# Kernel optimization log

Hardware: AMD Instinct MI355X
Metric: run time of the kernel (lower is better)

The kernel has to match this reference:

```python
import jax, jax.numpy as jnp
import numpy as np

N_NODES = 50000
N_EDGES = 600000
D = 128
EDGE_D = 32
N_LAYERS = 3
BN_EPS = 1e-5


def setup_inputs() -> dict:
    key = jax.random.key(0)
    ks = jax.random.split(key, 8)
    x = jax.random.normal(ks[0], (N_NODES, D), dtype=jnp.float32)
    edge_index = jax.random.randint(ks[1], (2, N_EDGES), 0, N_NODES, dtype=jnp.int64)
    edge_attr = jax.random.normal(ks[2], (N_EDGES, EDGE_D), dtype=jnp.float32)
    W_lin = jax.random.normal(ks[3], (N_LAYERS, EDGE_D, D), dtype=jnp.float32) * 0.05
    b_lin = jnp.zeros((N_LAYERS, D), dtype=jnp.float32)
    W1 = jax.random.normal(ks[4], (N_LAYERS, D, D), dtype=jnp.float32) * 0.05
    b1 = jnp.zeros((N_LAYERS, D), dtype=jnp.float32)
    W2 = jax.random.normal(ks[5], (N_LAYERS, D, D), dtype=jnp.float32) * 0.05
    b2 = jnp.zeros((N_LAYERS, D), dtype=jnp.float32)
    gamma = jnp.ones((N_LAYERS, D), dtype=jnp.float32)
    beta = jnp.zeros((N_LAYERS, D), dtype=jnp.float32)
    return {"x": x, "edge_index": edge_index, "edge_attr": edge_attr,
            "W_lin": W_lin, "b_lin": b_lin, "W1": W1, "b1": b1,
            "W2": W2, "b2": b2, "gamma": gamma, "beta": beta}


def reference(x, edge_index, edge_attr, W_lin, b_lin, W1, b1, W2, b2, gamma, beta):
    # MPNN with GINEConv layers: for each layer,
    #   msg_e = ReLU(x[src_e] + Linear(edge_attr_e))      (PyG GINEConv edge lift)
    #   agg_i = sum over edges with dst==i of msg_e        (scatter-sum)
    #   h     = MLP((1+eps)*x + agg), eps=0
    #   x     = ReLU(BatchNorm1d(h))                       (training-mode batch stats)
    src, dst = edge_index[0], edge_index[1]
    n = x.shape[0]
    for l in range(W1.shape[0]):
        e = edge_attr @ W_lin[l] + b_lin[l]                 # [E, D]
        msg = jax.nn.relu(x[src] + e)                       # gather + fuse
        agg = jax.ops.segment_sum(msg, dst, num_segments=n)  # [N, D]
        h = x + agg                                         # eps = 0
        h = jax.nn.relu(h @ W1[l] + b1[l]) @ W2[l] + b2[l]   # GIN MLP
        mu = jnp.mean(h, axis=0)
        var = jnp.var(h, axis=0)
        h = (h - mu) * jax.lax.rsqrt(var + BN_EPS) * gamma[l] + beta[l]
        x = jax.nn.relu(h)
    return x
```

## Files before the change

kernel.cpp:

```cpp
#include <hip/hip_runtime.h>

#define D_DIM 128
#define EDGE_DIM 32
#define BN_EPS 1e-5f

typedef __attribute__((ext_vector_type(8))) _Float16 f16x8;
typedef __attribute__((ext_vector_type(2))) _Float16 half2v;
typedef __attribute__((ext_vector_type(4))) float f32x4;
typedef unsigned short ushort_t;

__device__ __forceinline__ unsigned short f2h(float f) {
    union { _Float16 h; unsigned short u; } c;
    c.h = (_Float16)f;
    return c.u;
}
__device__ __forceinline__ unsigned pk2h(float lo, float hi) {
    return (unsigned)f2h(lo) | ((unsigned)f2h(hi) << 16);
}
__device__ __forceinline__ half2v asH2(unsigned u) {
    union { unsigned u; half2v h; } c;
    c.u = u;
    return c.h;
}
__device__ __forceinline__ float fdot2f(half2v a, half2v b, float c) {
#if __has_builtin(__builtin_amdgcn_fdot2)
    return __builtin_amdgcn_fdot2(a, b, c, false);
#else
    return c + (float)a.x * (float)b.x + (float)a.y * (float)b.y;
#endif
}

__global__ __launch_bounds__(256) void hist_kernel(
    const int* __restrict__ dst, int* __restrict__ cnt, int E)
{
    for (int e = blockIdx.x * 256 + threadIdx.x; e < E; e += gridDim.x * 256)
        atomicAdd(&cnt[dst[e]], 1);
}

__global__ __launch_bounds__(256) void scan_local_kernel(
    const int* __restrict__ cnt, int* __restrict__ off,
    int* __restrict__ blksum, int n)
{
    __shared__ int part[256];
    const int t = threadIdx.x;
    const int base = blockIdx.x * 2048 + t * 8;
    int v[8];
    int s = 0;
#pragma unroll
    for (int j = 0; j < 8; ++j) {
        const int idx = base + j;
        const int c = (idx < n) ? cnt[idx] : 0;
        v[j] = s;
        s += c;
    }
    part[t] = s;
    __syncthreads();
    for (int d = 1; d < 256; d <<= 1) {
        const int val = (t >= d) ? part[t - d] : 0;
        __syncthreads();
        part[t] += val;
        __syncthreads();
    }
    const int texcl = (t > 0) ? part[t - 1] : 0;
#pragma unroll
    for (int j = 0; j < 8; ++j) {
        const int idx = base + j;
        if (idx < n) off[idx] = texcl + v[j];
    }
    if (t == 255) blksum[blockIdx.x] = part[255];
}

__global__ __launch_bounds__(64) void scan_tops_kernel(
    int* __restrict__ blksum, int* __restrict__ off, int n, int B)
{
    if (threadIdx.x == 0) {
        int run = 0;
        for (int b = 0; b < B; ++b) {
            const int v = blksum[b];
            blksum[b] = run;
            run += v;
        }
        off[n] = run;
    }
}

__global__ __launch_bounds__(256) void scan_add_kernel(
    int* __restrict__ off, int* __restrict__ cur,
    const int* __restrict__ blksum, int n)
{
    const int base = blockIdx.x * 2048;
    const int add = blksum[blockIdx.x];
    for (int j = threadIdx.x; j < 2048; j += 256) {
        const int i = base + j;
        if (i < n) {
            const int v = off[i] + add;
            off[i] = v;
            cur[i] = v;
        }
    }
}

__global__ __launch_bounds__(256) void scatter_conv_kernel(
    const int* __restrict__ src, const int* __restrict__ dst,
    const float* __restrict__ ea,
    int* __restrict__ cur, int* __restrict__ srcs,
    uint4* __restrict__ ea16q, int E)
{
    for (int e = blockIdx.x * 256 + threadIdx.x; e < E; e += gridDim.x * 256) {
        const int p = atomicAdd(&cur[dst[e]], 1);
        srcs[p] = src[e];
        const float* __restrict__ er = ea + (size_t)e * EDGE_DIM;
#pragma unroll
        for (int q = 0; q < 4; ++q) {
            const float4 a = *(const float4*)(er + q * 8);
            const float4 b = *(const float4*)(er + q * 8 + 4);
            uint4 o;
            o.x = pk2h(a.x, a.y); o.y = pk2h(a.z, a.w);
            o.z = pk2h(b.x, b.y); o.w = pk2h(b.z, b.w);
            ea16q[(size_t)p * 4 + q] = o;
        }
    }
}

__global__ __launch_bounds__(256) void wl_build_kernel(
    const float* __restrict__ Wl, unsigned* __restrict__ wl16d)
{
#pragma unroll
    for (int r = 0; r < 8; ++r) {
        const int idx = r * 256 + threadIdx.x;
        const int kp = idx >> 7, c = idx & 127;
        wl16d[idx] = pk2h(Wl[(2 * kp) * D_DIM + c], Wl[(2 * kp + 1) * D_DIM + c]);
    }
}

__global__ __launch_bounds__(256) void xprep0_kernel(
    const float* __restrict__ h, uint2* __restrict__ x16q, int M)
{
    const int total = M * 32;
    for (int i = blockIdx.x * 256 + threadIdx.x; i < total; i += gridDim.x * 256) {
        const float4 v = ((const float4*)h)[i];
        uint2 o; o.x = pk2h(v.x, v.y); o.y = pk2h(v.z, v.w);
        x16q[i] = o;
    }
}

template<int OUTF32>
__global__ __launch_bounds__(256) void apply_kernel(
    const ushort_t* __restrict__ h16, const float* __restrict__ scsh,
    uint2* __restrict__ x16q, float* __restrict__ outp, int M)
{
    __shared__ float sc[128], sh[128];
    if (threadIdx.x < 128) {
        sc[threadIdx.x] = scsh[threadIdx.x];
        sh[threadIdx.x] = scsh[128 + threadIdx.x];
    }
    __syncthreads();
    const int total = M * 32;
    for (int i = blockIdx.x * 256 + threadIdx.x; i < total; i += gridDim.x * 256) {
        const uint2 hv = *(const uint2*)(h16 + (size_t)i * 4);
        const half2v a = asH2(hv.x), b = asH2(hv.y);
        const int c = (i & 31) * 4;
        const float v0 = fmaxf(fmaf((float)a.x, sc[c + 0], sh[c + 0]), 0.f);
        const float v1 = fmaxf(fmaf((float)a.y, sc[c + 1], sh[c + 1]), 0.f);
        const float v2 = fmaxf(fmaf((float)b.x, sc[c + 2], sh[c + 2]), 0.f);
        const float v3 = fmaxf(fmaf((float)b.y, sc[c + 3], sh[c + 3]), 0.f);
        if (OUTF32) {
            f32x4 o = {v0, v1, v2, v3};
            *(f32x4*)(outp + (size_t)i * 4) = o;
        } else {
            uint2 o; o.x = pk2h(v0, v1); o.y = pk2h(v2, v3);
            x16q[i] = o;
        }
    }
}

__global__ __launch_bounds__(256, 2) void edge_agg_kernel(
    const unsigned* __restrict__ x16d,
    const int*      __restrict__ srcs,
    const uint4*    __restrict__ ea16q,
    const int*      __restrict__ row_off,
    const unsigned* __restrict__ wl16d,
    const float*    __restrict__ bl,
    float*          __restrict__ agg,
    int nNodes)
{
    const int lane = threadIdx.x & 63;
    const int wid  = threadIdx.x >> 6;

    unsigned wA[16], wB[16];
#pragma unroll
    for (int kp = 0; kp < 16; ++kp) {
        const uint2 w2 = *(const uint2*)(wl16d + kp * 128 + 2 * lane);
        wA[kp] = w2.x; wB[kp] = w2.y;
    }
#pragma unroll
    for (int kp = 0; kp < 16; ++kp) {
        asm volatile("" : "+v"(wA[kp]));
        asm volatile("" : "+v"(wB[kp]));
    }
    const float b0 = bl[2 * lane];
    const float b1 = bl[2 * lane + 1];

    const int stride = gridDim.x * 4;
    for (int node = blockIdx.x * 4 + wid; node < nNodes; node += stride) {
        const int beg = __builtin_amdgcn_readfirstlane(row_off[node]);
        const int end = __builtin_amdgcn_readfirstlane(row_off[node + 1]);
        float acc0 = 0.f, acc1 = 0.f;

        const int nPair = (end - beg) >> 1;
        int j = beg;
        int sA = 0, sB = 0;
        if (nPair > 0) { sA = srcs[j]; sB = srcs[j + 1]; }

#pragma unroll 1
        for (int it = 0; it < nPair; ++it) {
            const unsigned xdA = x16d[(size_t)sA * 64 + lane];
            const unsigned xdB = x16d[(size_t)sB * 64 + lane];
            int sA2 = sA, sB2 = sB;
            if (it + 1 < nPair) {
                sA2 = srcs[j + 2];
                sB2 = srcs[j + 3];
            }
            const uint4 a0 = ea16q[(size_t)j * 4 + 0];
            const uint4 a1 = ea16q[(size_t)j * 4 + 1];
            const uint4 a2 = ea16q[(size_t)j * 4 + 2];
            const uint4 a3 = ea16q[(size_t)j * 4 + 3];
            const uint4 c0 = ea16q[(size_t)(j + 1) * 4 + 0];
            const uint4 c1 = ea16q[(size_t)(j + 1) * 4 + 1];
            const uint4 c2 = ea16q[(size_t)(j + 1) * 4 + 2];
            const uint4 c3 = ea16q[(size_t)(j + 1) * 4 + 3];

            const unsigned awA[16] = {a0.x, a0.y, a0.z, a0.w,
                                      a1.x, a1.y, a1.z, a1.w,
                                      a2.x, a2.y, a2.z, a2.w,
                                      a3.x, a3.y, a3.z, a3.w};
            const unsigned awB[16] = {c0.x, c0.y, c0.z, c0.w,
                                      c1.x, c1.y, c1.z, c1.w,
                                      c2.x, c2.y, c2.z, c2.w,
                                      c3.x, c3.y, c3.z, c3.w};
            float pA0 = b0, pA1 = b1, pB0 = b0, pB1 = b1;
            float qA0 = 0.f, qA1 = 0.f, qB0 = 0.f, qB1 = 0.f;
#pragma unroll
            for (int kp = 0; kp < 8; ++kp) {
                pA0 = fdot2f(asH2(awA[kp]), asH2(wA[kp]), pA0);
                pA1 = fdot2f(asH2(awA[kp]), asH2(wB[kp]), pA1);
                pB0 = fdot2f(asH2(awB[kp]), asH2(wA[kp]), pB0);
                pB1 = fdot2f(asH2(awB[kp]), asH2(wB[kp]), pB1);
                qA0 = fdot2f(asH2(awA[kp + 8]), asH2(wA[kp + 8]), qA0);
                qA1 = fdot2f(asH2(awA[kp + 8]), asH2(wB[kp + 8]), qA1);
                qB0 = fdot2f(asH2(awB[kp + 8]), asH2(wA[kp + 8]), qB0);
                qB1 = fdot2f(asH2(awB[kp + 8]), asH2(wB[kp + 8]), qB1);
            }
            const half2v xhA = asH2(xdA);
            const half2v xhB = asH2(xdB);
            acc0 += fmaxf((float)xhA.x + pA0 + qA0, 0.f)
                  + fmaxf((float)xhB.x + pB0 + qB0, 0.f);
            acc1 += fmaxf((float)xhA.y + pA1 + qA1, 0.f)
                  + fmaxf((float)xhB.y + pB1 + qB1, 0.f);
            sA = sA2; sB = sB2;
            j += 2;
        }
        if (j < end) {
            const int s = srcs[j];
            const unsigned xd = x16d[(size_t)s * 64 + lane];
            const uint4 a0 = ea16q[(size_t)j * 4 + 0];
            const uint4 a1 = ea16q[(size_t)j * 4 + 1];
            const uint4 a2 = ea16q[(size_t)j * 4 + 2];
            const uint4 a3 = ea16q[(size_t)j * 4 + 3];
            const unsigned aw[16] = {a0.x, a0.y, a0.z, a0.w,
                                     a1.x, a1.y, a1.z, a1.w,
                                     a2.x, a2.y, a2.z, a2.w,
                                     a3.x, a3.y, a3.z, a3.w};
            float p0 = b0, p1 = b1, q0 = 0.f, q1 = 0.f;
#pragma unroll
            for (int kp = 0; kp < 8; ++kp) {
                p0 = fdot2f(asH2(aw[kp]), asH2(wA[kp]), p0);
                p1 = fdot2f(asH2(aw[kp]), asH2(wB[kp]), p1);
                q0 = fdot2f(asH2(aw[kp + 8]), asH2(wA[kp + 8]), q0);
                q1 = fdot2f(asH2(aw[kp + 8]), asH2(wB[kp + 8]), q1);
            }
            const half2v xh = asH2(xd);
            acc0 += fmaxf((float)xh.x + p0 + q0, 0.f);
            acc1 += fmaxf((float)xh.y + p1 + q1, 0.f);
        }
        *(float2*)(agg + (size_t)node * D_DIM + 2 * lane) = make_float2(acc0, acc1);
    }
}

__global__ __launch_bounds__(256) void fused_mlp_kernel(
    const unsigned* __restrict__ x16d,
    const float* __restrict__ agg,
    const float* __restrict__ W1,
    const float* __restrict__ b1,
    const float* __restrict__ W2,
    const float* __restrict__ b2,
    ushort_t* __restrict__ h16,
    float* __restrict__ sums,
    int M)
{
    __shared__ char ATb[128 * 256];
    __shared__ char WTb[128 * 256];
    __shared__ float bsum[256];
    const int tid = threadIdx.x;
    const int m0  = blockIdx.x * 128;

    bsum[tid] = 0.f;

#pragma unroll
    for (int i = 0; i < 16; ++i) {
        const int idx = i * 256 + tid;
        const int r = idx >> 5, c4 = idx & 31;
        const int row = m0 + r;
        f32x4 v = {0.f, 0.f, 0.f, 0.f};
        if (row < M) {
            const uint2 xv = *(const uint2*)(x16d + (size_t)row * 64 + c4 * 2);
            const f32x4 g  = *(const f32x4*)(agg + (size_t)row * 128 + c4 * 4);
            const half2v xa = asH2(xv.x), xb = asH2(xv.y);
            v[0] = (float)xa.x + g[0];
            v[1] = (float)xa.y + g[1];
            v[2] = (float)xb.x + g[2];
            v[3] = (float)xb.y + g[3];
        }
        uint2 p; p.x = pk2h(v[0], v[1]); p.y = pk2h(v[2], v[3]);
        *(uint2*)(ATb + r * 256 + ((c4 * 8) ^ ((r & 7) << 4))) = p;
    }
#pragma unroll
    for (int i = 0; i < 8; ++i) {
        const int c4 = (tid >> 6) + 4 * i;
        const int kp = tid & 63;
        const f32x4 wa = *(const f32x4*)(W1 + (size_t)(2 * kp) * 128 + c4 * 4);
        const f32x4 wb = *(const f32x4*)(W1 + (size_t)(2 * kp + 1) * 128 + c4 * 4);
#pragma unroll
        for (int j = 0; j < 4; ++j) {
            const int col = c4 * 4 + j;
            *(unsigned*)(WTb + col * 256 + ((kp * 4) ^ ((col & 7) << 4))) = pk2h(wa[j], wb[j]);
        }
    }
    __syncthreads();

    const int lane = tid & 63;
    const int w    = tid >> 6;
    const int fr   = lane & 15;
    const int fg   = lane >> 4;
    const int ar0  = w * 32 + fr;
    const int asz  = (ar0 & 7) << 4;

    f32x4 acc[2][8];
#pragma unroll
    for (int a = 0; a < 2; ++a)
#pragma unroll
        for (int b = 0; b < 8; ++b) acc[a][b] = (f32x4){0.f, 0.f, 0.f, 0.f};

#pragma unroll
    for (int ks = 0; ks < 4; ++ks) {
        const int kb = ks * 64 + fg * 16;
        const f16x8 a0 = *(const f16x8*)(ATb + ar0 * 256 + (kb ^ asz));
        const f16x8 a1 = *(const f16x8*)(ATb + (ar0 + 16) * 256 + (kb ^ asz));
#pragma unroll
        for (int cb = 0; cb < 8; ++cb) {
            const int col = cb * 16 + fr;
            const f16x8 b = *(const f16x8*)(WTb + col * 256 + (kb ^ ((col & 7) << 4)));
            acc[0][cb] = __builtin_amdgcn_mfma_f32_16x16x32_f16(a0, b, acc[0][cb], 0, 0, 0);
            acc[1][cb] = __builtin_amdgcn_mfma_f32_16x16x32_f16(a1, b, acc[1][cb], 0, 0, 0);
        }
    }
    __syncthreads();

    {
        float b1v[8];
#pragma unroll
        for (int cb = 0; cb < 8; ++cb) b1v[cb] = b1[cb * 16 + fr];
#pragma unroll
        for (int rf = 0; rf < 2; ++rf) {
            const int rb = w * 32 + rf * 16 + fg * 4;
#pragma unroll
            for (int cb = 0; cb < 8; ++cb) {
                const int c = cb * 16 + fr;
#pragma unroll
                for (int j = 0; j < 4; ++j) {
                    const int r = rb + j;
                    const float v = fmaxf(acc[rf][cb][j] + b1v[cb], 0.f);
                    *(ushort_t*)(ATb + r * 256 + ((c * 2) ^ ((r & 7) << 4))) = f2h(v);
                }
            }
        }
    }
#pragma unroll
    for (int i = 0; i < 8; ++i) {
        const int c4 = (tid >> 6) + 4 * i;
        const int kp = tid & 63;
        const f32x4 wa = *(const f32x4*)(W2 + (size_t)(2 * kp) * 128 + c4 * 4);
        const f32x4 wb = *(const f32x4*)(W2 + (size_t)(2 * kp + 1) * 128 + c4 * 4);
#pragma unroll
        for (int j = 0; j < 4; ++j) {
            const int col = c4 * 4 + j;
            *(unsigned*)(WTb + col * 256 + ((kp * 4) ^ ((col & 7) << 4))) = pk2h(wa[j], wb[j]);
        }
    }
#pragma unroll
    for (int a = 0; a < 2; ++a)
#pragma unroll
        for (int b = 0; b < 8; ++b) acc[a][b] = (f32x4){0.f, 0.f, 0.f, 0.f};
    __syncthreads();

#pragma unroll
    for (int ks = 0; ks < 4; ++ks) {
        const int kb = ks * 64 + fg * 16;
        const f16x8 a0 = *(const f16x8*)(ATb + ar0 * 256 + (kb ^ asz));
        const f16x8 a1 = *(const f16x8*)(ATb + (ar0 + 16) * 256 + (kb ^ asz));
#pragma unroll
        for (int cb = 0; cb < 8; ++cb) {
            const int col = cb * 16 + fr;
            const f16x8 b = *(const f16x8*)(WTb + col * 256 + (kb ^ ((col & 7) << 4)));
            acc[0][cb] = __builtin_amdgcn_mfma_f32_16x16x32_f16(a0, b, acc[0][cb], 0, 0, 0);
            acc[1][cb] = __builtin_amdgcn_mfma_f32_16x16x32_f16(a1, b, acc[1][cb], 0, 0, 0);
        }
    }

    float b2v[8];
#pragma unroll
    for (int cb = 0; cb < 8; ++cb) b2v[cb] = b2[cb * 16 + fr];
    float s[8], q[8];
#pragma unroll
    for (int cb = 0; cb < 8; ++cb) { s[cb] = 0.f; q[cb] = 0.f; }

#pragma unroll
    for (int rf = 0; rf < 2; ++rf) {
        const int r0 = m0 + w * 32 + rf * 16 + fg * 4;
#pragma unroll
        for (int cb = 0; cb < 8; ++cb) {
            const int col = cb * 16 + fr;
#pragma unroll
            for (int j = 0; j < 4; ++j) {
                const int row = r0 + j;
                if (row < M) {
                    const float v = acc[rf][cb][j] + b2v[cb];
                    h16[(size_t)row * 128 + col] = f2h(v);
                    s[cb] += v;
                    q[cb] += v * v;
                }
            }
        }
    }
#pragma unroll
    for (int cb = 0; cb < 8; ++cb) {
        float ss = s[cb]; ss += __shfl_down(ss, 32); ss += __shfl_down(ss, 16);
        float qq = q[cb]; qq += __shfl_down(qq, 32); qq += __shfl_down(qq, 16);
        if (lane < 16) {
            atomicAdd(&bsum[cb * 16 + lane], ss);
            atomicAdd(&bsum[128 + cb * 16 + lane], qq);
        }
    }
    __syncthreads();
    unsafeAtomicAdd(&sums[tid], bsum[tid]);
}

__global__ __launch_bounds__(128) void bn_finalize_kernel(
    const float* __restrict__ sums,
    const float* __restrict__ gamma, const float* __restrict__ beta,
    float* __restrict__ scsh, float invM)
{
    const int c = threadIdx.x;
    const float mu  = sums[c] * invM;
    const float var = sums[128 + c] * invM - mu * mu;
    const float sc  = gamma[c] * rsqrtf(var + BN_EPS);
    scsh[c]       = sc;
    scsh[128 + c] = beta[c] - mu * sc;
}

extern "C" void kernel_launch(void* const* d_in, const int* in_sizes, int n_in,
                              void* d_out, int out_size, void* d_ws, size_t ws_size,
                              hipStream_t stream)
{
    const float* x_in  = (const float*)d_in[0];
    const int*   ei    = (const int*)  d_in[1];
    const float* ea    = (const float*)d_in[2];
    const float* W_lin = (const float*)d_in[3];
    const float* b_lin = (const float*)d_in[4];
    const float* W1    = (const float*)d_in[5];
    const float* b1    = (const float*)d_in[6];
    const float* W2    = (const float*)d_in[7];
    const float* b2    = (const float*)d_in[8];
    const float* gamma = (const float*)d_in[9];
    const float* beta  = (const float*)d_in[10];

    const int N = in_sizes[0] / D_DIM;
    const int E = in_sizes[2] / EDGE_DIM;
    const int L = in_sizes[3] / (EDGE_DIM * D_DIM);

    const int* src = ei;
    const int* dst = ei + E;

    float* out = (float*)d_out;

    char* wp = (char*)d_ws;
    auto take = [&wp](size_t bytes) {
        char* r = wp;
        wp += (bytes + 15) & ~(size_t)15;
        return r;
    };
    float*     agg     = (float*)    take((size_t)N * D_DIM * 4);
    ushort_t*  h16     = (ushort_t*) take((size_t)N * D_DIM * 2);
    unsigned*  x16d    = (unsigned*) take((size_t)N * D_DIM * 2);
    float*     sums    = (float*)    take(256 * 4);
    float*     scsh    = (float*)    take(256 * 4);
    unsigned*  wl16d   = (unsigned*) take(16 * 128 * 4);
    int*       cnt     = (int*)      take((size_t)N * 4);
    int*       row_off = (int*)      take((size_t)(N + 1) * 4);
    int*       cur     = (int*)      take((size_t)N * 4);
    int*       blksum  = (int*)      take(256 * 4);
    int*       srcs    = (int*)      take((size_t)E * 4);
    uint4*     ea16q   = (uint4*)    take((size_t)E * 64);

    const int gemmBlocks = (N + 127) / 128;
    const int scanBlocks = (N + 2047) / 2048;

    hipMemsetAsync(cnt, 0, (size_t)N * sizeof(int), stream);
    hist_kernel<<<1024, 256, 0, stream>>>(dst, cnt, E);
    scan_local_kernel<<<scanBlocks, 256, 0, stream>>>(cnt, row_off, blksum, N);
    scan_tops_kernel<<<1, 64, 0, stream>>>(blksum, row_off, N, scanBlocks);
    scan_add_kernel<<<scanBlocks, 256, 0, stream>>>(row_off, cur, blksum, N);
    scatter_conv_kernel<<<1024, 256, 0, stream>>>(src, dst, ea, cur, srcs, ea16q, E);

    for (int l = 0; l < L; ++l) {
        hipMemsetAsync(sums, 0, 256 * sizeof(float), stream);

        const float* Wl_l = W_lin + (size_t)l * EDGE_DIM * D_DIM;
        const float* bl_l = b_lin + (size_t)l * D_DIM;
        const float* W1_l = W1 + (size_t)l * D_DIM * D_DIM;
        const float* b1_l = b1 + (size_t)l * D_DIM;
        const float* W2_l = W2 + (size_t)l * D_DIM * D_DIM;
        const float* b2_l = b2 + (size_t)l * D_DIM;

        if (l == 0)
            xprep0_kernel<<<1024, 256, 0, stream>>>(x_in, (uint2*)x16d, N);
        else
            apply_kernel<0><<<1024, 256, 0, stream>>>(h16, scsh, (uint2*)x16d, nullptr, N);

        wl_build_kernel<<<1, 256, 0, stream>>>(Wl_l, wl16d);

        edge_agg_kernel<<<2048, 256, 0, stream>>>(
            x16d, srcs, ea16q, row_off, wl16d, bl_l, agg, N);

        fused_mlp_kernel<<<gemmBlocks, 256, 0, stream>>>(
            x16d, agg, W1_l, b1_l, W2_l, b2_l, h16, sums, N);

        bn_finalize_kernel<<<1, 128, 0, stream>>>(
            sums, gamma + (size_t)l * D_DIM, beta + (size_t)l * D_DIM,
            scsh, 1.f / (float)N);
    }

    apply_kernel<1><<<1024, 256, 0, stream>>>(h16, scsh, nullptr, out, N);
}
```

Baseline: 428.3 us.

## Fuse residual add into edge aggregation, store fp16, prebuild MLP weights once

The edge aggregation kernel now adds the node's own features and writes the sum as fp16, which halves the agg buffer traffic and removes the separate x+agg pass in the MLP kernel. The W1/W2 fp16 transposes move into a single weight-build kernel run once per layer. The MLP kernel then reads B fragments straight from global memory (L2-resident) instead of staging them through shared memory per block. This cuts per-block conversion work and LDS usage. The cost is an fp16 rounding of x+agg and uncoalesced global weight loads inside the MFMA loop.

```diff
diff --git a/kernel.cpp b/kernel.cpp
--- a/kernel.cpp
+++ b/kernel.cpp
@@ -122,14 +122,24 @@
     }
 }
 
-__global__ __launch_bounds__(256) void wl_build_kernel(
-    const float* __restrict__ Wl, unsigned* __restrict__ wl16d)
-{
-#pragma unroll
-    for (int r = 0; r < 8; ++r) {
-        const int idx = r * 256 + threadIdx.x;
+__global__ __launch_bounds__(256) void wbuild_kernel(
+    const float* __restrict__ Wl, const float* __restrict__ W1f,
+    const float* __restrict__ W2f,
+    unsigned* __restrict__ wl16d, unsigned* __restrict__ wf1d,
+    unsigned* __restrict__ wf2d)
+{
+    const int idx = blockIdx.x * 256 + threadIdx.x;
+    if (idx < 2048) {
         const int kp = idx >> 7, c = idx & 127;
         wl16d[idx] = pk2h(Wl[(2 * kp) * D_DIM + c], Wl[(2 * kp + 1) * D_DIM + c]);
+    } else if (idx < 10240) {
+        const int i = idx - 2048;
+        const int col = i >> 6, kp = i & 63;
+        wf1d[i] = pk2h(W1f[(2 * kp) * D_DIM + col], W1f[(2 * kp + 1) * D_DIM + col]);
+    } else if (idx < 18432) {
+        const int i = idx - 10240;
+        const int col = i >> 6, kp = i & 63;
+        wf2d[i] = pk2h(W2f[(2 * kp) * D_DIM + col], W2f[(2 * kp + 1) * D_DIM + col]);
     }
 }
 
@@ -181,7 +191,7 @@
     const int*      __restrict__ row_off,
     const unsigned* __restrict__ wl16d,
     const float*    __restrict__ bl,
-    float*          __restrict__ agg,
+    unsigned*       __restrict__ agg16d,
     int nNodes)
 {
     const int lane = threadIdx.x & 63;
@@ -283,23 +293,23 @@
             acc0 += fmaxf((float)xh.x + p0 + q0, 0.f);
             acc1 += fmaxf((float)xh.y + p1 + q1, 0.f);
         }
-        *(float2*)(agg + (size_t)node * D_DIM + 2 * lane) = make_float2(acc0, acc1);
+        const half2v xo = asH2(x16d[(size_t)node * 64 + lane]);
+        agg16d[(size_t)node * 64 + lane] =
+            pk2h((float)xo.x + acc0, (float)xo.y + acc1);
     }
 }
 
 __global__ __launch_bounds__(256) void fused_mlp_kernel(
-    const unsigned* __restrict__ x16d,
-    const float* __restrict__ agg,
-    const float* __restrict__ W1,
+    const unsigned* __restrict__ agg16d,
+    const ushort_t* __restrict__ wf1,
     const float* __restrict__ b1,
-    const float* __restrict__ W2,
+    const ushort_t* __restrict__ wf2,
     const float* __restrict__ b2,
     ushort_t* __restrict__ h16,
     float* __restrict__ sums,
     int M)
 {
     __shared__ char ATb[128 * 256];
-    __shared__ char WTb[128 * 256];
     __shared__ float bsum[256];
     const int tid = threadIdx.x;
     const int m0  = blockIdx.x * 128;
@@ -307,34 +317,13 @@
     bsum[tid] = 0.f;
 
 #pragma unroll
-    for (int i = 0; i < 16; ++i) {
+    for (int i = 0; i < 8; ++i) {
         const int idx = i * 256 + tid;
-        const int r = idx >> 5, c4 = idx & 31;
+        const int r = idx >> 4, c16 = idx & 15;
         const int row = m0 + r;
-        f32x4 v = {0.f, 0.f, 0.f, 0.f};
-        if (row < M) {
-            const uint2 xv = *(const uint2*)(x16d + (size_t)row * 64 + c4 * 2);
-            const f32x4 g  = *(const f32x4*)(agg + (size_t)row * 128 + c4 * 4);
-            const half2v xa = asH2(xv.x), xb = asH2(xv.y);
-            v[0] = (float)xa.x + g[0];
-            v[1] = (float)xa.y + g[1];
-            v[2] = (float)xb.x + g[2];
-            v[3] = (float)xb.y + g[3];
-        }
-        uint2 p; p.x = pk2h(v[0], v[1]); p.y = pk2h(v[2], v[3]);
-        *(uint2*)(ATb + r * 256 + ((c4 * 8) ^ ((r & 7) << 4))) = p;
-    }
-#pragma unroll
-    for (int i = 0; i < 8; ++i) {
-        const int c4 = (tid >> 6) + 4 * i;
-        const int kp = tid & 63;
-        const f32x4 wa = *(const f32x4*)(W1 + (size_t)(2 * kp) * 128 + c4 * 4);
-        const f32x4 wb = *(const f32x4*)(W1 + (size_t)(2 * kp + 1) * 128 + c4 * 4);
-#pragma unroll
-        for (int j = 0; j < 4; ++j) {
-            const int col = c4 * 4 + j;
-            *(unsigned*)(WTb + col * 256 + ((kp * 4) ^ ((col & 7) << 4))) = pk2h(wa[j], wb[j]);
-        }
+        uint4 v = make_uint4(0u, 0u, 0u, 0u);
+        if (row < M) v = *(const uint4*)(agg16d + (size_t)row * 64 + c16 * 4);
+        *(uint4*)(ATb + r * 256 + ((c16 * 16) ^ ((r & 7) << 4))) = v;
     }
     __syncthreads();
 
@@ -356,12 +345,16 @@
         const int kb = ks * 64 + fg * 16;
         const f16x8 a0 = *(const f16x8*)(ATb + ar0 * 256 + (kb ^ asz));
         const f16x8 a1 = *(const f16x8*)(ATb + (ar0 + 16) * 256 + (kb ^ asz));
+        f16x8 bfr[8];
 #pragma unroll
         for (int cb = 0; cb < 8; ++cb) {
             const int col = cb * 16 + fr;
-            const f16x8 b = *(const f16x8*)(WTb + col * 256 + (kb ^ ((col & 7) << 4)));
-            acc[0][cb] = __builtin_amdgcn_mfma_f32_16x16x32_f16(a0, b, acc[0][cb], 0, 0, 0);
-            acc[1][cb] = __builtin_amdgcn_mfma_f32_16x16x32_f16(a1, b, acc[1][cb], 0, 0, 0);
+            bfr[cb] = *(const f16x8*)(wf1 + col * 128 + ks * 32 + fg * 8);
+        }
+#pragma unroll
+        for (int cb = 0; cb < 8; ++cb) {
+            acc[0][cb] = __builtin_amdgcn_mfma_f32_16x16x32_f16(a0, bfr[cb], acc[0][cb], 0, 0, 0);
+            acc[1][cb] = __builtin_amdgcn_mfma_f32_16x16x32_f16(a1, bfr[cb], acc[1][cb], 0, 0, 0);
         }
     }
     __syncthreads();
@@ -386,18 +379,6 @@
         }
     }
 #pragma unroll
-    for (int i = 0; i < 8; ++i) {
-        const int c4 = (tid >> 6) + 4 * i;
-        const int kp = tid & 63;
-        const f32x4 wa = *(const f32x4*)(W2 + (size_t)(2 * kp) * 128 + c4 * 4);
-        const f32x4 wb = *(const f32x4*)(W2 + (size_t)(2 * kp + 1) * 128 + c4 * 4);
-#pragma unroll
-        for (int j = 0; j < 4; ++j) {
-            const int col = c4 * 4 + j;
-            *(unsigned*)(WTb + col * 256 + ((kp * 4) ^ ((col & 7) << 4))) = pk2h(wa[j], wb[j]);
-        }
-    }
-#pragma unroll
     for (int a = 0; a < 2; ++a)
 #pragma unroll
         for (int b = 0; b < 8; ++b) acc[a][b] = (f32x4){0.f, 0.f, 0.f, 0.f};
@@ -408,12 +389,16 @@
         const int kb = ks * 64 + fg * 16;
         const f16x8 a0 = *(const f16x8*)(ATb + ar0 * 256 + (kb ^ asz));
         const f16x8 a1 = *(const f16x8*)(ATb + (ar0 + 16) * 256 + (kb ^ asz));
+        f16x8 bfr[8];
 #pragma unroll
         for (int cb = 0; cb < 8; ++cb) {
             const int col = cb * 16 + fr;
-            const f16x8 b = *(const f16x8*)(WTb + col * 256 + (kb ^ ((col & 7) << 4)));
-            acc[0][cb] = __builtin_amdgcn_mfma_f32_16x16x32_f16(a0, b, acc[0][cb], 0, 0, 0);
-            acc[1][cb] = __builtin_amdgcn_mfma_f32_16x16x32_f16(a1, b, acc[1][cb], 0, 0, 0);
+            bfr[cb] = *(const f16x8*)(wf2 + col * 128 + ks * 32 + fg * 8);
+        }
+#pragma unroll
+        for (int cb = 0; cb < 8; ++cb) {
+            acc[0][cb] = __builtin_amdgcn_mfma_f32_16x16x32_f16(a0, bfr[cb], acc[0][cb], 0, 0, 0);
+            acc[1][cb] = __builtin_amdgcn_mfma_f32_16x16x32_f16(a1, bfr[cb], acc[1][cb], 0, 0, 0);
         }
     }
 
@@ -499,12 +484,14 @@
         wp += (bytes + 15) & ~(size_t)15;
         return r;
     };
-    float*     agg     = (float*)    take((size_t)N * D_DIM * 4);
+    unsigned*  agg16d  = (unsigned*) take((size_t)N * D_DIM * 2);
     ushort_t*  h16     = (ushort_t*) take((size_t)N * D_DIM * 2);
     unsigned*  x16d    = (unsigned*) take((size_t)N * D_DIM * 2);
     float*     sums    = (float*)    take(256 * 4);
     float*     scsh    = (float*)    take(256 * 4);
     unsigned*  wl16d   = (unsigned*) take(16 * 128 * 4);
+    unsigned*  wf1d    = (unsigned*) take(128 * 64 * 4);
+    unsigned*  wf2d    = (unsigned*) take(128 * 64 * 4);
     int*       cnt     = (int*)      take((size_t)N * 4);
     int*       row_off = (int*)      take((size_t)(N + 1) * 4);
     int*       cur     = (int*)      take((size_t)N * 4);
@@ -537,13 +524,14 @@
         else
             apply_kernel<0><<<1024, 256, 0, stream>>>(h16, scsh, (uint2*)x16d, nullptr, N);
 
-        wl_build_kernel<<<1, 256, 0, stream>>>(Wl_l, wl16d);
+        wbuild_kernel<<<72, 256, 0, stream>>>(Wl_l, W1_l, W2_l, wl16d, wf1d, wf2d);
 
         edge_agg_kernel<<<2048, 256, 0, stream>>>(
-            x16d, srcs, ea16q, row_off, wl16d, bl_l, agg, N);
+            x16d, srcs, ea16q, row_off, wl16d, bl_l, agg16d, N);
 
         fused_mlp_kernel<<<gemmBlocks, 256, 0, stream>>>(
-            x16d, agg, W1_l, b1_l, W2_l, b2_l, h16, sums, N);
+            agg16d, (const ushort_t*)wf1d, b1_l,
+            (const ushort_t*)wf2d, b2_l, h16, sums, N);
 
         bn_finalize_kernel<<<1, 128, 0, stream>>>(
             sums, gamma + (size_t)l * D_DIM, beta + (size_t)l * D_DIM,
```

After: 439.3 us. 1.03x slower.
